# Kernel tuning notes

Hardware: AMD Instinct MI355X
Metric: run time of the kernel (lower is better)

## Reference

```python
import jax, jax.numpy as jnp
import numpy as np

EPS = 1e-5
DN = ('NCHW', 'OIHW', 'NCHW')


def _conv3x3(x, w):
    return jax.lax.conv_general_dilated(x, w, (1, 1), 'SAME', dimension_numbers=DN)


def _bn_relu(x, g, b):
    # eval-mode BN: running_mean=0, running_var=1
    scale = (g / jnp.sqrt(1.0 + EPS))[None, :, None, None]
    return jax.nn.relu(x * scale + b[None, :, None, None])


def _double_conv(x, w1, g1, b1, w2, g2, b2):
    x = _bn_relu(_conv3x3(x, w1), g1, b1)
    return _bn_relu(_conv3x3(x, w2), g2, b2)


def _up2x_bilinear_align(x):
    # bilinear, align_corners=True, scale_factor=2
    def interp(a, axis, n_in):
        n_out = 2 * n_in
        pos = jnp.arange(n_out, dtype=jnp.float32) * (n_in - 1) / (n_out - 1)
        lo = jnp.floor(pos).astype(jnp.int32)
        hi = jnp.minimum(lo + 1, n_in - 1)
        w = pos - lo.astype(jnp.float32)
        sh = [1, 1, 1, 1]
        sh[axis] = n_out
        w = w.reshape(sh)
        return jnp.take(a, lo, axis=axis) * (1.0 - w) + jnp.take(a, hi, axis=axis) * w
    B, C, H, W = x.shape
    return interp(interp(x, 2, H), 3, W)


def _lstm_dir(seq, Wih, Whh, bih, bhh, reverse):
    # seq: (N, T, C) -> (N, T, Hh); PyTorch gate order i,f,g,o
    Hh = Whh.shape[1]
    xg = jnp.einsum('ntc,gc->ntg', seq, Wih) + (bih + bhh)
    if reverse:
        xg = xg[:, ::-1]
    xg = jnp.swapaxes(xg, 0, 1)  # (T, N, 4H)
    N = seq.shape[0]
    h0 = jnp.zeros((N, Hh), seq.dtype)

    def step(carry, gx):
        h, c = carry
        g = gx + h @ Whh.T
        i, f, gg, o = jnp.split(g, 4, axis=-1)
        c = jax.nn.sigmoid(f) * c + jax.nn.sigmoid(i) * jnp.tanh(gg)
        h = jax.nn.sigmoid(o) * jnp.tanh(c)
        return (h, c), h

    _, hs = jax.lax.scan(step, (h0, h0), xg)
    hs = jnp.swapaxes(hs, 0, 1)  # (N, T, Hh)
    if reverse:
        hs = hs[:, ::-1]
    return hs


def _bilstm(seq, Wf, Uf, bif, bhf, Wb, Ub, bib, bhb):
    return jnp.concatenate([
        _lstm_dir(seq, Wf, Uf, bif, bhf, False),
        _lstm_dir(seq, Wb, Ub, bib, bhb, True),
    ], axis=-1)


def _site_rows(x, lstm):
    # batched version of per-row LSTM: each row is a sequence over W, features C
    B, C, H, W = x.shape
    s = jnp.transpose(x, (0, 2, 3, 1)).reshape(B * H, W, C)
    out = _bilstm(s, *lstm)  # (B*H, W, C) since 2*hidden == C
    return jnp.transpose(out.reshape(B, H, W, C), (0, 3, 1, 2))


def _site_cols(x, lstm):
    # each column is a sequence over H, features C
    B, C, H, W = x.shape
    s = jnp.transpose(x, (0, 3, 2, 1)).reshape(B * W, H, C)
    out = _bilstm(s, *lstm)
    return jnp.transpose(out.reshape(B, W, H, C), (0, 3, 2, 1))


def setup_inputs() -> dict:
    key = jax.random.key(0)
    ks = jax.random.split(key, 24)
    d = {}
    d['x1'] = jax.random.normal(ks[0], (8, 128, 32, 32), jnp.float32)
    d['x2'] = jax.random.normal(ks[1], (8, 128, 64, 64), jnp.float32)
    # bidirectional LSTM: input 256, hidden 128
    d['lstm_Wih_f'] = jax.random.normal(ks[2], (512, 256), jnp.float32) * 0.06
    d['lstm_Whh_f'] = jax.random.normal(ks[3], (512, 128), jnp.float32) * 0.08
    d['lstm_bih_f'] = jax.random.normal(ks[4], (512,), jnp.float32) * 0.05
    d['lstm_bhh_f'] = jax.random.normal(ks[5], (512,), jnp.float32) * 0.05
    d['lstm_Wih_b'] = jax.random.normal(ks[6], (512, 256), jnp.float32) * 0.06
    d['lstm_Whh_b'] = jax.random.normal(ks[7], (512, 128), jnp.float32) * 0.08
    d['lstm_bib_tmp'] = None
    del d['lstm_bib_tmp']
    d['lstm_bih_b'] = jax.random.normal(ks[8], (512,), jnp.float32) * 0.05
    d['lstm_bhh_b'] = jax.random.normal(ks[9], (512,), jnp.float32) * 0.05
    # conv_2 = DoubleConv(512, 256) (mid=256), shared across its two call sites
    d['c2_w1'] = jax.random.normal(ks[10], (256, 512, 3, 3), jnp.float32) * 0.02
    d['c2_g1'] = jax.random.uniform(ks[11], (256,), jnp.float32, 0.5, 1.5)
    d['c2_b1'] = jax.random.normal(ks[12], (256,), jnp.float32) * 0.05
    d['c2_w2'] = jax.random.normal(ks[13], (256, 256, 3, 3), jnp.float32) * 0.03
    d['c2_g2'] = jax.random.uniform(ks[14], (256,), jnp.float32, 0.5, 1.5)
    d['c2_b2'] = jax.random.normal(ks[15], (256,), jnp.float32) * 0.05
    # conv = DoubleConv(256, 128, mid=128)
    d['cv_w1'] = jax.random.normal(ks[16], (128, 256, 3, 3), jnp.float32) * 0.03
    d['cv_g1'] = jax.random.uniform(ks[17], (128,), jnp.float32, 0.5, 1.5)
    d['cv_b1'] = jax.random.normal(ks[18], (128,), jnp.float32) * 0.05
    d['cv_w2'] = jax.random.normal(ks[19], (128, 128, 3, 3), jnp.float32) * 0.04
    d['cv_g2'] = jax.random.uniform(ks[20], (128,), jnp.float32, 0.5, 1.5)
    d['cv_b2'] = jax.random.normal(ks[21], (128,), jnp.float32) * 0.05
    return d


def reference(x1, x2, lstm_Wih_f, lstm_Whh_f, lstm_bih_f, lstm_bhh_f,
              lstm_Wih_b, lstm_Whh_b, lstm_bih_b, lstm_bhh_b,
              c2_w1, c2_g1, c2_b1, c2_w2, c2_g2, c2_b2,
              cv_w1, cv_g1, cv_b1, cv_w2, cv_g2, cv_b2):
    lstm = (lstm_Wih_f, lstm_Whh_f, lstm_bih_f, lstm_bhh_f,
            lstm_Wih_b, lstm_Whh_b, lstm_bih_b, lstm_bhh_b)
    x1u = _up2x_bilinear_align(x1)
    dy = x2.shape[2] - x1u.shape[2]
    dx = x2.shape[3] - x1u.shape[3]
    x1u = jnp.pad(x1u, ((0, 0), (0, 0), (dy // 2, dy - dy // 2), (dx // 2, dx - dx // 2)))
    x = jnp.concatenate([x2, x1u], axis=1)  # (B, 256, 64, 64)
    # site_relation mutates x in-place in torch: rows pass, then cols pass on the
    # row-updated tensor; x_weigth and x_heigth alias the same final tensor.
    x = _site_rows(x, lstm)
    x = _site_cols(x, lstm)
    x_site = jnp.concatenate([x, x], axis=1)  # (B, 512, H, W)
    x_site = _double_conv(x_site, c2_w1, c2_g1, c2_b1, c2_w2, c2_g2, c2_b2)
    x = jnp.concatenate([x, x_site], axis=1)  # (B, 512, H, W)
    x = _double_conv(x, c2_w1, c2_g1, c2_b1, c2_w2, c2_g2, c2_b2)
    x = _double_conv(x, cv_w1, cv_g1, cv_b1, cv_w2, cv_g2, cv_b2)
    return x  # (B, 128, 64, 64)
```

## Files before the change

### kernel.cpp

```cpp
#include <hip/hip_runtime.h>
#include <hip/hip_bf16.h>
#include <math.h>

typedef __bf16 bf16x8 __attribute__((ext_vector_type(8)));
typedef float  f32x4  __attribute__((ext_vector_type(4)));

__device__ __forceinline__ float sigm(float x)  { return 1.f/(1.f+__expf(-x)); }
__device__ __forceinline__ float tanh_f(float x){ return 2.f/(1.f+__expf(-2.f*x)) - 1.f; }
__device__ __forceinline__ float b2f(unsigned short u){
  unsigned int x = ((unsigned int)u) << 16; return __uint_as_float(x);
}
__device__ __forceinline__ unsigned short f2b(float v){
  __hip_bfloat16 h = __float2bfloat16(v); return *(unsigned short*)&h;
}
__device__ __forceinline__ void glds16(const void* g, void* l) {
  __builtin_amdgcn_global_load_lds(
      (const __attribute__((address_space(1))) unsigned int*)g,
      (__attribute__((address_space(3))) unsigned int*)l, 16, 0, 0);
}
__device__ __forceinline__ bf16x8 bzero() {
  bf16x8 v;
  #pragma unroll
  for (int i = 0; i < 8; ++i) v[i] = (__bf16)0.0f;
  return v;
}
__device__ __forceinline__ void barrier_lds() {
  asm volatile("s_waitcnt lgkmcnt(0)\n\ts_barrier" ::: "memory");
}

__global__ __launch_bounds__(256) void k_upcat(const float* __restrict__ x1,
                                               const float* __restrict__ x2,
                                               __hip_bfloat16* __restrict__ X0) {
  int idx = blockIdx.x*256 + threadIdx.x;
  int c = idx & 255;
  int w = (idx >> 8) & 63;
  int h = (idx >> 14) & 63;
  int n = idx >> 20;
  float v;
  if (c < 128) {
    v = x2[((n*128 + c)*64 + h)*64 + w];
  } else {
    int cc = c - 128;
    float py = (h*31.0f)/63.0f;
    int ly = (int)py; int hy = min(ly+1, 31); float fy = py - (float)ly;
    float px = (w*31.0f)/63.0f;
    int lx = (int)px; int hx = min(lx+1, 31); float fx = px - (float)lx;
    const float* p = x1 + (size_t)(n*128 + cc)*1024;
    float v00 = p[ly*32+lx], v01 = p[ly*32+hx];
    float v10 = p[hy*32+lx], v11 = p[hy*32+hx];
    v = (1.f-fy)*((1.f-fx)*v00 + fx*v01) + fy*((1.f-fx)*v10 + fx*v11);
  }
  X0[idx] = __float2bfloat16(v);
}

__global__ __launch_bounds__(256) void k_wih_prep(
    const float* __restrict__ Wf, const float* __restrict__ Wb,
    const float* __restrict__ bif, const float* __restrict__ bhf,
    const float* __restrict__ bib, const float* __restrict__ bhb,
    __hip_bfloat16* __restrict__ wihc, float* __restrict__ biasc) {
  int idx = blockIdx.x*256 + threadIdx.x;
  int n = idx >> 8, k = idx & 255;
  float v = (n < 512) ? Wf[n*256 + k] : Wb[(n-512)*256 + k];
  wihc[idx] = __float2bfloat16(v);
  if (idx < 1024) biasc[idx] = (idx < 512) ? bif[idx] + bhf[idx]
                                           : bib[idx-512] + bhb[idx-512];
}

__global__ __launch_bounds__(256) void k_xg_gemm(
    const __hip_bfloat16* __restrict__ Xin,
    const __hip_bfloat16* __restrict__ Wihc,
    const float* __restrict__ biasc,
    __hip_bfloat16* __restrict__ xg) {
  __shared__ __align__(16) unsigned short sa[128][72];
  __shared__ __align__(16) unsigned short sw[128][72];
  int bx = blockIdx.x;
  int t = bx >> 2, seq0 = (bx & 3) << 7;
  int n0 = blockIdx.y << 7;
  int tid = threadIdx.x, lane = tid & 63, wid = tid >> 6;
  int wm = wid >> 1, wn = wid & 1;
  int l15 = lane & 15, quad = lane >> 4;
  f32x4 acc[4][4];
  #pragma unroll
  for (int i = 0; i < 4; ++i)
    #pragma unroll
    for (int j = 0; j < 4; ++j) acc[i][j] = (f32x4){0.f,0.f,0.f,0.f};

  for (int k0 = 0; k0 < 256; k0 += 64) {
    __syncthreads();
    for (int idx = tid; idx < 2048; idx += 256) {
      int row = idx >> 4, c4 = (idx & 15) << 2;
      *(ushort4*)&sa[row][c4] = *(const ushort4*)((const unsigned short*)Xin +
          (size_t)((seq0 + row)*64 + t)*256 + k0 + c4);
      *(ushort4*)&sw[row][c4] = *(const ushort4*)((const unsigned short*)Wihc +
          (size_t)(n0 + row)*256 + k0 + c4);
    }
    __syncthreads();
    #pragma unroll
    for (int k32 = 0; k32 < 64; k32 += 32) {
      bf16x8 af[4], bfr[4];
      #pragma unroll
      for (int mt = 0; mt < 4; ++mt)
        af[mt] = *(const bf16x8*)&sa[wm*64 + mt*16 + l15][k32 + quad*8];
      #pragma unroll
      for (int nt = 0; nt < 4; ++nt)
        bfr[nt] = *(const bf16x8*)&sw[wn*64 + nt*16 + l15][k32 + quad*8];
      #pragma unroll
      for (int mt = 0; mt < 4; ++mt)
        #pragma unroll
        for (int nt = 0; nt < 4; ++nt)
          acc[mt][nt] = __builtin_amdgcn_mfma_f32_16x16x32_bf16(
              af[mt], bfr[nt], acc[mt][nt], 0, 0, 0);
    }
  }
  #pragma unroll
  for (int nt = 0; nt < 4; ++nt) {
    int cg = n0 + wn*64 + nt*16 + l15;
    int dir = cg >> 9;
    int g   = (cg >> 7) & 3;
    int u   = cg & 127;
    float bias = biasc[cg];
    unsigned short* op = (unsigned short*)xg +
        (size_t)(((dir*64 + t)*4 + g)*512)*128 + u;
    #pragma unroll
    for (int mt = 0; mt < 4; ++mt) {
      int sbase = seq0 + wm*64 + mt*16 + quad*4;
      f32x4 a = acc[mt][nt];
      #pragma unroll
      for (int r = 0; r < 4; ++r)
        op[(size_t)(sbase + r)*128] = f2b(a[r] + bias);
    }
  }
}

__global__ __launch_bounds__(256, 2) void k_lstm_rec(
    const __hip_bfloat16* __restrict__ xg,
    const float* __restrict__ WhhF, const float* __restrict__ WhhB,
    __hip_bfloat16* __restrict__ out) {
  const int dir = blockIdx.y;
  const int sb  = blockIdx.x;
  const float* Whh = dir ? WhhB : WhhF;
  __shared__ __align__(16) unsigned short hs[16][136];
  __shared__ __align__(16) float gv[2][128][4];
  const int tid = threadIdx.x, lane = tid & 63, wv = tid >> 6;
  const int l15 = lane & 15, quad = lane >> 4;

  bf16x8 wf[4][2][4];
  #pragma unroll
  for (int g = 0; g < 4; ++g)
    #pragma unroll
    for (int ut = 0; ut < 2; ++ut) {
      int gate = g*128 + wv*32 + ut*16 + l15;
      #pragma unroll
      for (int kc = 0; kc < 4; ++kc) {
        const float* wp = Whh + (size_t)gate*128 + kc*32 + quad*8;
        float4 w0 = *(const float4*)wp;
        float4 w1 = *(const float4*)(wp + 4);
        bf16x8 f;
        f[0]=(__bf16)w0.x; f[1]=(__bf16)w0.y; f[2]=(__bf16)w0.z; f[3]=(__bf16)w0.w;
        f[4]=(__bf16)w1.x; f[5]=(__bf16)w1.y; f[6]=(__bf16)w1.z; f[7]=(__bf16)w1.w;
        wf[g][ut][kc] = f;
      }
    }
  for (int i = tid; i < 16*136; i += 256) ((unsigned short*)hs)[i] = 0;

  const int u_ = tid & 127;
  const int s_ = tid >> 7;
  float cst = 0.f;

  const unsigned short* xp = (const unsigned short*)xg +
      (size_t)dir*64*4*512*128;
  unsigned short xv[4], xn[4];
  #define LDX(stp, dst)                                                    \
    {                                                                      \
      int ts_ = (stp) < 64 ? (stp) : 63;                                   \
      int t_  = dir ? 63 - ts_ : ts_;                                      \
      _Pragma("unroll")                                                    \
      for (int g_ = 0; g_ < 4; ++g_)                                       \
        dst[g_] = xp[(size_t)((t_*4 + g_)*512 + sb*2 + s_)*128 + u_];      \
    }
  LDX(0, xv);
  __syncthreads();

  for (int step = 0; step < 64; ++step) {
    int t = dir ? 63 - step : step;
    LDX(step + 1, xn);
    bf16x8 af[4];
    #pragma unroll
    for (int kc = 0; kc < 4; ++kc)
      af[kc] = *(const bf16x8*)&hs[l15][kc*32 + quad*8];
    f32x4 acc[4][2];
    #pragma unroll
    for (int g = 0; g < 4; ++g)
      #pragma unroll
      for (int ut = 0; ut < 2; ++ut) acc[g][ut] = (f32x4){0.f,0.f,0.f,0.f};
    #pragma unroll
    for (int kc = 0; kc < 4; ++kc)
      #pragma unroll
      for (int g = 0; g < 4; ++g)
        #pragma unroll
        for (int ut = 0; ut < 2; ++ut)
          acc[g][ut] = __builtin_amdgcn_mfma_f32_16x16x32_bf16(
              af[kc], wf[g][ut][kc], acc[g][ut], 0, 0, 0);
    if (quad == 0) {
      #pragma unroll
      for (int ut = 0; ut < 2; ++ut) {
        int u = wv*32 + ut*16 + l15;
        #pragma unroll
        for (int r = 0; r < 2; ++r) {
          float4 q;
          q.x = acc[0][ut][r]; q.y = acc[1][ut][r];
          q.z = acc[2][ut][r]; q.w = acc[3][ut][r];
          *(float4*)&gv[r][u][0] = q;
        }
      }
    }
    barrier_lds();
    {
      float4 gq = *(const float4*)&gv[s_][u_][0];
      float I = gq.x + b2f(xv[0]);
      float F = gq.y + b2f(xv[1]);
      float G = gq.z + b2f(xv[2]);
      float O = gq.w + b2f(xv[3]);
      float cv = sigm(F)*cst + sigm(I)*tanh_f(G);
      float hv = sigm(O)*tanh_f(cv);
      cst = cv;
      unsigned short hb = f2b(hv);
      hs[s_][u_] = hb;
      int gs = sb*2 + s_;
      ((unsigned short*)out)[(size_t)(((gs >> 6)*64 + t)*64 + (gs & 63))*256
                             + dir*128 + u_] = hb;
    }
    barrier_lds();
    #pragma unroll
    for (int g = 0; g < 4; ++g) xv[g] = xn[g];
  }
  #undef LDX
}

__global__ __launch_bounds__(256) void k_wrefmt_bf16(const float* __restrict__ src,
                                                     __hip_bfloat16* __restrict__ dst,
                                                     int Ci, int Co, int fold) {
  int idx = blockIdx.x*256 + threadIdx.x;
  int total = 9*Ci*Co;
  if (idx >= total) return;
  int ci = idx % Ci;
  int co = (idx / Ci) % Co;
  int k  = idx / (Ci*Co);
  int CiS = fold ? Ci*2 : Ci;
  float v = src[(size_t)(co*CiS + ci)*9 + k];
  if (fold) v += src[(size_t)(co*CiS + ci + Ci)*9 + k];
  dst[idx] = __float2bfloat16(v);
}

__global__ __launch_bounds__(256, 2) void k_conv3_v2(
    const __hip_bfloat16* __restrict__ inA, const __hip_bfloat16* __restrict__ inB,
    const __hip_bfloat16* __restrict__ wgt,
    const float* __restrict__ gam, const float* __restrict__ bet,
    float* __restrict__ outF, __hip_bfloat16* __restrict__ outB,
    int Cin, int Co, int nchw) {
  __shared__ __align__(16) unsigned short si[2][64][64];
  __shared__ __align__(16) unsigned short sw[3][128][64];
  int bx = blockIdx.x;
  int n  = bx >> 5;
  int h0 = (bx & 31) << 1;
  int co0 = blockIdx.y << 7;
  int tid = threadIdx.x;
  int lane = tid & 63;
  int wid  = tid >> 6;
  int wm = wid >> 1;
  int wn = wid & 1;
  int l15 = lane & 15, quad = lane >> 4;

  f32x4 acc[4][4];
  #pragma unroll
  for (int i = 0; i < 4; ++i)
    #pragma unroll
    for (int j = 0; j < 4; ++j) acc[i][j] = (f32x4){0.f,0.f,0.f,0.f};

  int cs = inB ? 256 : Cin;
  for (int ky = 0; ky < 3; ++ky) {
    for (int ci0 = 0; ci0 < Cin; ci0 += 64) {
      const unsigned short* src = (const unsigned short*)inA; int cb = ci0;
      if (inB && ci0 >= 256) { src = (const unsigned short*)inB; cb = ci0 - 256; }
      __syncthreads();
      {
        int r = wid >> 1;
        int ih = h0 + r + ky - 1;
        int half = (wid & 1) << 5;
        if (ih >= 0 && ih <= 63) {
          const unsigned short* gsrc = src + (size_t)((n*64 + ih)*64)*cs + cb;
          int pl = lane >> 3, pc = lane & 7;
          #pragma unroll
          for (int q = 0; q < 4; ++q) {
            int iw = half + q*8 + pl;
            int lc = pc ^ (iw & 7);
            glds16(gsrc + (size_t)iw*cs + lc*8, &si[r][half + q*8][0]);
          }
        } else {
          uint4 z = {0,0,0,0};
          #pragma unroll
          for (int q = 0; q < 4; ++q)
            *(uint4*)(&si[r][half + q*8][0] + lane*8) = z;
        }
      }
      {
        int col = lane >> 3, pc = lane & 7;
        const unsigned short* wk = (const unsigned short*)wgt +
            (size_t)(ky*3*Co + co0)*Cin + ci0;
        #pragma unroll
        for (int j = 0; j < 12; ++j) {
          int s = wid + j*4;
          int kx = s >> 4, co8 = (s & 15) << 3;
          int co = co8 + col;
          int lc = pc ^ (co & 7);
          glds16(wk + (size_t)(kx*Co + co)*Cin + lc*8, &sw[kx][co8][0]);
        }
      }
      __syncthreads();
      #pragma unroll
      for (int kx = 0; kx < 3; ++kx) {
        #pragma unroll
        for (int k32 = 0; k32 < 2; ++k32) {
          bf16x8 af[4], bfr[4];
          #pragma unroll
          for (int mt = 0; mt < 4; ++mt) {
            int iw = mt*16 + l15 + kx - 1;
            int iwc = iw & 63;
            int pc = (k32*4 + quad) ^ (iwc & 7);
            af[mt] = *(const bf16x8*)&si[wm][iwc][pc*8];
            if ((kx == 0 && mt == 0 && l15 == 0) ||
                (kx == 2 && mt == 3 && l15 == 15))
              af[mt] = bzero();
          }
          #pragma unroll
          for (int nt = 0; nt < 4; ++nt) {
            int co = wn*64 + nt*16 + l15;
            int pc = (k32*4 + quad) ^ (co & 7);
            bfr[nt] = *(const bf16x8*)&sw[kx][co][pc*8];
          }
          #pragma unroll
          for (int mt = 0; mt < 4; ++mt)
            #pragma unroll
            for (int nt = 0; nt < 4; ++nt)
              acc[mt][nt] = __builtin_amdgcn_mfma_f32_16x16x32_bf16(
                  af[mt], bfr[nt], acc[mt][nt], 0, 0, 0);
        }
      }
    }
  }
  const float kS = 0.9999950000374997f;
  int h = h0 + wm;
  #pragma unroll
  for (int nt = 0; nt < 4; ++nt) {
    int co = co0 + wn*64 + nt*16 + l15;
    float scale = gam[co]*kS, bb = bet[co];
    #pragma unroll
    for (int mt = 0; mt < 4; ++mt) {
      f32x4 a = acc[mt][nt];
      #pragma unroll
      for (int r = 0; r < 4; ++r) {
        int w = mt*16 + quad*4 + r;
        float v = fmaf(a[r], scale, bb);
        v = v > 0.f ? v : 0.f;
        if (nchw) outF[(size_t)((n*Co + co)*64 + h)*64 + w] = v;
        else      outB[(size_t)((n*64 + h)*64 + w)*Co + co] = __float2bfloat16(v);
      }
    }
  }
}

extern "C" void kernel_launch(void* const* d_in, const int* in_sizes, int n_in,
                              void* d_out, int out_size, void* d_ws, size_t ws_size,
                              hipStream_t stream) {
  const float* x1    = (const float*)d_in[0];
  const float* x2    = (const float*)d_in[1];
  const float* Wih_f = (const float*)d_in[2];
  const float* Whh_f = (const float*)d_in[3];
  const float* bih_f = (const float*)d_in[4];
  const float* bhh_f = (const float*)d_in[5];
  const float* Wih_b = (const float*)d_in[6];
  const float* Whh_b = (const float*)d_in[7];
  const float* bih_b = (const float*)d_in[8];
  const float* bhh_b = (const float*)d_in[9];
  const float* c2_w1 = (const float*)d_in[10];
  const float* c2_g1 = (const float*)d_in[11];
  const float* c2_b1 = (const float*)d_in[12];
  const float* c2_w2 = (const float*)d_in[13];
  const float* c2_g2 = (const float*)d_in[14];
  const float* c2_b2 = (const float*)d_in[15];
  const float* cv_w1 = (const float*)d_in[16];
  const float* cv_g1 = (const float*)d_in[17];
  const float* cv_b1 = (const float*)d_in[18];
  const float* cv_w2 = (const float*)d_in[19];
  const float* cv_g2 = (const float*)d_in[20];
  const float* cv_b2 = (const float*)d_in[21];

  char* base = (char*)d_ws;
  const size_t SLOTB = 16777216ull;
  __hip_bfloat16* Xb  = (__hip_bfloat16*)(base);
  __hip_bfloat16* Sb  = (__hip_bfloat16*)(base);
  __hip_bfloat16* XG  = (__hip_bfloat16*)(base + SLOTB);
  __hip_bfloat16* D2  = (__hip_bfloat16*)(base + SLOTB);
  __hip_bfloat16* D2b = (__hip_bfloat16*)(base + 2*SLOTB);
  __hip_bfloat16* RT  = (__hip_bfloat16*)(base + SLOTB + 67108864ull);
  __hip_bfloat16* D1  = RT;
  char* wq = base + SLOTB + 67108864ull + SLOTB;
  __hip_bfloat16* wihc  = (__hip_bfloat16*)wq;
  float*          biasc = (float*)(wq + 524288);
  char* cw = wq + 528384;
  __hip_bfloat16* w1f    = (__hip_bfloat16*)(cw);
  __hip_bfloat16* w1full = (__hip_bfloat16*)(cw + 1179648);
  __hip_bfloat16* w2r    = (__hip_bfloat16*)(cw + 3538944);
  __hip_bfloat16* wv1    = (__hip_bfloat16*)(cw + 4718592);
  __hip_bfloat16* wv2    = (__hip_bfloat16*)(cw + 5308416);

  k_wih_prep<<<1024, 256, 0, stream>>>(Wih_f, Wih_b, bih_f, bhh_f, bih_b, bhh_b,
                                       wihc, biasc);
  k_wrefmt_bf16<<<(9*256*256+255)/256, 256, 0, stream>>>(c2_w1, w1f,    256, 256, 1);
  k_wrefmt_bf16<<<(9*512*256+255)/256, 256, 0, stream>>>(c2_w1, w1full, 512, 256, 0);
  k_wrefmt_bf16<<<(9*256*256+255)/256, 256, 0, stream>>>(c2_w2, w2r,    256, 256, 0);
  k_wrefmt_bf16<<<(9*256*128+255)/256, 256, 0, stream>>>(cv_w1, wv1,    256, 128, 0);
  k_wrefmt_bf16<<<(9*128*128+255)/256, 256, 0, stream>>>(cv_w2, wv2,    128, 128, 0);

  k_upcat<<<32768, 256, 0, stream>>>(x1, x2, Xb);

  k_xg_gemm<<<dim3(256, 8), 256, 0, stream>>>(Xb, wihc, biasc, XG);
  k_lstm_rec<<<dim3(256, 2), 256, 0, stream>>>(XG, Whh_f, Whh_b, RT);
  k_xg_gemm<<<dim3(256, 8), 256, 0, stream>>>(RT, wihc, biasc, XG);
  k_lstm_rec<<<dim3(256, 2), 256, 0, stream>>>(XG, Whh_f, Whh_b, Sb);

  k_conv3_v2<<<dim3(256,2), 256, 0, stream>>>(Sb, nullptr, w1f, c2_g1, c2_b1,
                                              nullptr, D1, 256, 256, 0);
  k_conv3_v2<<<dim3(256,2), 256, 0, stream>>>(D1, nullptr, w2r, c2_g2, c2_b2,
                                              nullptr, D2, 256, 256, 0);
  k_conv3_v2<<<dim3(256,2), 256, 0, stream>>>(Sb, D2, w1full, c2_g1, c2_b1,
                                              nullptr, D2b, 512, 256, 0);
  k_conv3_v2<<<dim3(256,2), 256, 0, stream>>>(D2b, nullptr, w2r, c2_g2, c2_b2,
                                              nullptr, D1, 256, 256, 0);
  k_conv3_v2<<<dim3(256,1), 256, 0, stream>>>(D1, nullptr, wv1, cv_g1, cv_b1,
                                              nullptr, D2, 256, 128, 0);
  k_conv3_v2<<<dim3(256,1), 256, 0, stream>>>(D2, nullptr, wv2, cv_g2, cv_b2,
                                              (float*)d_out, nullptr, 128, 128, 1);
}
```

Measured before the change: 664.1 us.

## Restructure LSTM recurrence to 16 sequences per block with in-register gates

New measurement: 734.5 us. 10.6% more time.

```diff
diff --git a/kernel.cpp b/kernel.cpp
--- a/kernel.cpp
+++ b/kernel.cpp
@@ -120,115 +120,93 @@
     int u   = cg & 127;
     float bias = biasc[cg];
     unsigned short* op = (unsigned short*)xg +
-        (size_t)(((dir*64 + t)*4 + g)*512)*128 + u;
+        ((size_t)((dir*64 + t)*4 + g)*128 + u)*512;
     #pragma unroll
     for (int mt = 0; mt < 4; ++mt) {
       int sbase = seq0 + wm*64 + mt*16 + quad*4;
       f32x4 a = acc[mt][nt];
-      #pragma unroll
-      for (int r = 0; r < 4; ++r)
-        op[(size_t)(sbase + r)*128] = f2b(a[r] + bias);
-    }
-  }
-}
-
-__global__ __launch_bounds__(256, 2) void k_lstm_rec(
+      ushort4 o;
+      o.x = f2b(a[0] + bias); o.y = f2b(a[1] + bias);
+      o.z = f2b(a[2] + bias); o.w = f2b(a[3] + bias);
+      *(ushort4*)(op + sbase) = o;
+    }
+  }
+}
+
+__global__ __launch_bounds__(512, 1) void k_lstm_rec(
     const __hip_bfloat16* __restrict__ xg,
     const float* __restrict__ WhhF, const float* __restrict__ WhhB,
     __hip_bfloat16* __restrict__ out) {
   const int dir = blockIdx.y;
   const int sb  = blockIdx.x;
   const float* Whh = dir ? WhhB : WhhF;
-  __shared__ __align__(16) unsigned short hs[16][136];
-  __shared__ __align__(16) float gv[2][128][4];
-  const int tid = threadIdx.x, lane = tid & 63, wv = tid >> 6;
+  __shared__ __align__(16) unsigned short hs[2][16][132];
+  const int tid = threadIdx.x, lane = tid & 63, w = tid >> 6;
   const int l15 = lane & 15, quad = lane >> 4;
-
-  bf16x8 wf[4][2][4];
+  const int u = w*16 + l15;
+
+  bf16x8 wf[4][4];
   #pragma unroll
   for (int g = 0; g < 4; ++g)
     #pragma unroll
-    for (int ut = 0; ut < 2; ++ut) {
-      int gate = g*128 + wv*32 + ut*16 + l15;
-      #pragma unroll
-      for (int kc = 0; kc < 4; ++kc) {
-        const float* wp = Whh + (size_t)gate*128 + kc*32 + quad*8;
-        float4 w0 = *(const float4*)wp;
-        float4 w1 = *(const float4*)(wp + 4);
-        bf16x8 f;
-        f[0]=(__bf16)w0.x; f[1]=(__bf16)w0.y; f[2]=(__bf16)w0.z; f[3]=(__bf16)w0.w;
-        f[4]=(__bf16)w1.x; f[5]=(__bf16)w1.y; f[6]=(__bf16)w1.z; f[7]=(__bf16)w1.w;
-        wf[g][ut][kc] = f;
-      }
-    }
-  for (int i = tid; i < 16*136; i += 256) ((unsigned short*)hs)[i] = 0;
-
-  const int u_ = tid & 127;
-  const int s_ = tid >> 7;
-  float cst = 0.f;
+    for (int kc = 0; kc < 4; ++kc) {
+      const float* wp = Whh + (size_t)(g*128 + u)*128 + kc*32 + quad*8;
+      float4 w0 = *(const float4*)wp;
+      float4 w1 = *(const float4*)(wp + 4);
+      bf16x8 f;
+      f[0]=(__bf16)w0.x; f[1]=(__bf16)w0.y; f[2]=(__bf16)w0.z; f[3]=(__bf16)w0.w;
+      f[4]=(__bf16)w1.x; f[5]=(__bf16)w1.y; f[6]=(__bf16)w1.z; f[7]=(__bf16)w1.w;
+      wf[g][kc] = f;
+    }
+  for (int i = tid; i < 2*16*132; i += 512) ((unsigned short*)hs)[i] = 0;
+
+  float cst[4] = {0.f, 0.f, 0.f, 0.f};
 
   const unsigned short* xp = (const unsigned short*)xg +
-      (size_t)dir*64*4*512*128;
-  unsigned short xv[4], xn[4];
-  #define LDX(stp, dst)                                                    \
-    {                                                                      \
-      int ts_ = (stp) < 64 ? (stp) : 63;                                   \
-      int t_  = dir ? 63 - ts_ : ts_;                                      \
-      _Pragma("unroll")                                                    \
-      for (int g_ = 0; g_ < 4; ++g_)                                       \
-        dst[g_] = xp[(size_t)((t_*4 + g_)*512 + sb*2 + s_)*128 + u_];      \
+      (size_t)dir*64*4*128*512 + sb*16 + quad*4;
+  ushort4 xv[4], xn[4];
+  #define LDX(stp, dst)                                                      \
+    {                                                                        \
+      int ts_ = (stp) < 64 ? (stp) : 63;                                     \
+      int t_  = dir ? 63 - ts_ : ts_;                                        \
+      _Pragma("unroll")                                                      \
+      for (int g_ = 0; g_ < 4; ++g_)                                         \
+        dst[g_] = *(const ushort4*)(xp + ((size_t)(t_*4 + g_)*128 + u)*512); \
     }
   LDX(0, xv);
   __syncthreads();
 
   for (int step = 0; step < 64; ++step) {
     int t = dir ? 63 - step : step;
+    int p = step & 1;
+    bf16x8 af[4];
+    #pragma unroll
+    for (int kc = 0; kc < 4; ++kc)
+      af[kc] = *(const bf16x8*)&hs[p][l15][kc*32 + quad*8];
+    f32x4 acc[4];
+    #pragma unroll
+    for (int g = 0; g < 4; ++g) {
+      acc[g][0] = b2f(xv[g].x); acc[g][1] = b2f(xv[g].y);
+      acc[g][2] = b2f(xv[g].z); acc[g][3] = b2f(xv[g].w);
+    }
     LDX(step + 1, xn);
-    bf16x8 af[4];
     #pragma unroll
     for (int kc = 0; kc < 4; ++kc)
-      af[kc] = *(const bf16x8*)&hs[l15][kc*32 + quad*8];
-    f32x4 acc[4][2];
-    #pragma unroll
-    for (int g = 0; g < 4; ++g)
-      #pragma unroll
-      for (int ut = 0; ut < 2; ++ut) acc[g][ut] = (f32x4){0.f,0.f,0.f,0.f};
-    #pragma unroll
-    for (int kc = 0; kc < 4; ++kc)
       #pragma unroll
       for (int g = 0; g < 4; ++g)
-        #pragma unroll
-        for (int ut = 0; ut < 2; ++ut)
-          acc[g][ut] = __builtin_amdgcn_mfma_f32_16x16x32_bf16(
-              af[kc], wf[g][ut][kc], acc[g][ut], 0, 0, 0);
-    if (quad == 0) {
-      #pragma unroll
-      for (int ut = 0; ut < 2; ++ut) {
-        int u = wv*32 + ut*16 + l15;
-        #pragma unroll
-        for (int r = 0; r < 2; ++r) {
-          float4 q;
-          q.x = acc[0][ut][r]; q.y = acc[1][ut][r];
-          q.z = acc[2][ut][r]; q.w = acc[3][ut][r];
-          *(float4*)&gv[r][u][0] = q;
-        }
-      }
-    }
-    barrier_lds();
-    {
-      float4 gq = *(const float4*)&gv[s_][u_][0];
-      float I = gq.x + b2f(xv[0]);
-      float F = gq.y + b2f(xv[1]);
-      float G = gq.z + b2f(xv[2]);
-      float O = gq.w + b2f(xv[3]);
-      float cv = sigm(F)*cst + sigm(I)*tanh_f(G);
+        acc[g] = __builtin_amdgcn_mfma_f32_16x16x32_bf16(
+            af[kc], wf[g][kc], acc[g], 0, 0, 0);
+    #pragma unroll
+    for (int r = 0; r < 4; ++r) {
+      float I = acc[0][r], F = acc[1][r], G = acc[2][r], O = acc[3][r];
+      float cv = sigm(F)*cst[r] + sigm(I)*tanh_f(G);
       float hv = sigm(O)*tanh_f(cv);
-      cst = cv;
+      cst[r] = cv;
       unsigned short hb = f2b(hv);
-      hs[s_][u_] = hb;
-      int gs = sb*2 + s_;
+      hs[1 - p][quad*4 + r][u] = hb;
+      int gs = sb*16 + quad*4 + r;
       ((unsigned short*)out)[(size_t)(((gs >> 6)*64 + t)*64 + (gs & 63))*256
-                             + dir*128 + u_] = hb;
+                             + dir*128 + u] = hb;
     }
     barrier_lds();
     #pragma unroll
@@ -425,9 +403,9 @@
   k_upcat<<<32768, 256, 0, stream>>>(x1, x2, Xb);
 
   k_xg_gemm<<<dim3(256, 8), 256, 0, stream>>>(Xb, wihc, biasc, XG);
-  k_lstm_rec<<<dim3(256, 2), 256, 0, stream>>>(XG, Whh_f, Whh_b, RT);
+  k_lstm_rec<<<dim3(32, 2), 512, 0, stream>>>(XG, Whh_f, Whh_b, RT);
   k_xg_gemm<<<dim3(256, 8), 256, 0, stream>>>(RT, wihc, biasc, XG);
-  k_lstm_rec<<<dim3(256, 2), 256, 0, stream>>>(XG, Whh_f, Whh_b, Sb);
+  k_lstm_rec<<<dim3(32, 2), 512, 0, stream>>>(XG, Whh_f, Whh_b, Sb);
 
   k_conv3_v2<<<dim3(256,2), 256, 0, stream>>>(Sb, nullptr, w1f, c2_g1, c2_b1,
                                               nullptr, D1, 256, 256, 0);
```
